# Kernel optimization log

Hardware: AMD Instinct MI355X
Metric: run time of the kernel (lower is better)

## Reference

```python
import jax, jax.numpy as jnp
import numpy as np

B, S, L, F, CD, NH, E, HID = 4, 1024, 256, 512, 768, 8, 8, 2048


def _xavier(k, shape):
    std = float(np.sqrt(1.0 / (shape[-2] + shape[-1])))
    return jax.random.normal(k, shape, dtype=jnp.float32) * std


def setup_inputs() -> dict:
    key = jax.random.key(0)
    ks = iter(jax.random.split(key, 64))
    nk = lambda: next(ks)
    inp = {}
    inp['x_r'] = jax.random.normal(nk(), (B, S, F), jnp.float32)
    inp['x_i'] = jax.random.normal(nk(), (B, S, F), jnp.float32)
    inp['ctx_r'] = jax.random.normal(nk(), (B, L, CD), jnp.float32)
    inp['ctx_i'] = jax.random.normal(nk(), (B, L, CD), jnp.float32)
    inp['ln1_g'] = jnp.ones((F,), jnp.float32)
    inp['ln2_g'] = jnp.ones((F,), jnp.float32)
    inp['ln3_g'] = jnp.ones((F,), jnp.float32)
    for pref, shp in [('sa_q', (F, F)), ('sa_k', (F, F)), ('sa_v', (F, F)), ('sa_o', (F, F)),
                      ('ca_q', (F, F)), ('ca_k', (CD, F)), ('ca_v', (CD, F)), ('ca_o', (F, F))]:
        inp[pref + 'Wr'] = _xavier(nk(), shp)
        inp[pref + 'Wi'] = _xavier(nk(), shp)
        inp[pref + 'br'] = jnp.zeros((F,), jnp.float32)
        inp[pref + 'bi'] = jnp.zeros((F,), jnp.float32)
    inp['moe_W1r'] = _xavier(nk(), (E, F, HID))
    inp['moe_W1i'] = _xavier(nk(), (E, F, HID))
    inp['moe_b1r'] = jnp.zeros((E, HID), jnp.float32)
    inp['moe_b1i'] = jnp.zeros((E, HID), jnp.float32)
    inp['moe_mb'] = jnp.zeros((E, HID), jnp.float32)  # modReLU bias
    inp['moe_W2r'] = _xavier(nk(), (E, HID, F))
    inp['moe_W2i'] = _xavier(nk(), (E, HID, F))
    inp['moe_b2r'] = jnp.zeros((E, F), jnp.float32)
    inp['moe_b2i'] = jnp.zeros((E, F), jnp.float32)
    return inp


def _clin(xr, xi, Wr, Wi, br, bi):
    # (xr + i xi) @ (Wr + i Wi) + (br + i bi)
    return xr @ Wr - xi @ Wi + br, xr @ Wi + xi @ Wr + bi


def _cln(xr, xi, g, eps=1e-6):
    amp = jnp.sqrt(xr * xr + xi * xi + eps)
    s = g * (amp / (jnp.mean(amp, axis=-1, keepdims=True) + eps)) / (amp + eps)
    return xr * s, xi * s


def _modrelu(xr, xi, b, eps=1e-10):
    amp = jnp.sqrt(xr * xr + xi * xi + eps)
    s = jax.nn.relu(amp + b) / (amp + eps)
    return xr * s, xi * s


def _cattn(xr, xi, cr, ci, qWr, qWi, qbr, qbi, kWr, kWi, kbr, kbi,
           vWr, vWi, vbr, vbi, oWr, oWi, obr, obi, nh):
    qr, qi = _clin(xr, xi, qWr, qWi, qbr, qbi)
    kr, ki = _clin(cr, ci, kWr, kWi, kbr, kbi)
    vr, vi = _clin(cr, ci, vWr, vWi, vbr, vbi)
    Bt, Sq, Ft = qr.shape
    Sk = kr.shape[1]
    d = Ft // nh
    sp = lambda t: t.reshape(Bt, t.shape[1], nh, d).transpose(0, 2, 1, 3)  # b n s d
    Qr, Qi, Kr, Ki, Vr, Vi = sp(qr), sp(qi), sp(kr), sp(ki), sp(vr), sp(vi)
    scale = 1.0 / float(d) ** 0.5
    scores = (jnp.einsum('bnqd,bnkd->bnqk', Qr, Kr)
              + jnp.einsum('bnqd,bnkd->bnqk', Qi, Ki)) * scale
    w = jax.nn.softmax(scores, axis=-1)
    mix = lambda t: jnp.einsum('bnqk,bnkd->bnqd', w, t).transpose(0, 2, 1, 3).reshape(Bt, Sq, Ft)
    return _clin(mix(Vr), mix(Vi), oWr, oWi, obr, obi)


def reference(x_r, x_i, ctx_r, ctx_i, ln1_g, ln2_g, ln3_g,
              sa_qWr, sa_qWi, sa_qbr, sa_qbi, sa_kWr, sa_kWi, sa_kbr, sa_kbi,
              sa_vWr, sa_vWi, sa_vbr, sa_vbi, sa_oWr, sa_oWi, sa_obr, sa_obi,
              ca_qWr, ca_qWi, ca_qbr, ca_qbi, ca_kWr, ca_kWi, ca_kbr, ca_kbi,
              ca_vWr, ca_vWi, ca_vbr, ca_vbi, ca_oWr, ca_oWi, ca_obr, ca_obi,
              moe_W1r, moe_W1i, moe_b1r, moe_b1i, moe_mb,
              moe_W2r, moe_W2i, moe_b2r, moe_b2i):
    # self-attention block
    hr, hi = _cln(x_r, x_i, ln1_g)
    ar, ai = _cattn(hr, hi, hr, hi, sa_qWr, sa_qWi, sa_qbr, sa_qbi,
                    sa_kWr, sa_kWi, sa_kbr, sa_kbi, sa_vWr, sa_vWi, sa_vbr, sa_vbi,
                    sa_oWr, sa_oWi, sa_obr, sa_obi, NH)
    xr, xi = x_r + ar, x_i + ai
    # cross-attention block
    hr, hi = _cln(xr, xi, ln2_g)
    ar, ai = _cattn(hr, hi, ctx_r, ctx_i, ca_qWr, ca_qWi, ca_qbr, ca_qbi,
                    ca_kWr, ca_kWi, ca_kbr, ca_kbi, ca_vWr, ca_vWi, ca_vbr, ca_vbi,
                    ca_oWr, ca_oWi, ca_obr, ca_obi, NH)
    xr, xi = xr + ar, xi + ai
    # phase-routed MoE block
    hr, hi = _cln(xr, xi, ln3_g)
    phase = jnp.arctan2(hi, hr)
    token_phase = jnp.arctan2(jnp.mean(jnp.sin(phase), axis=-1),
                              jnp.mean(jnp.cos(phase), axis=-1))
    idx = jnp.clip(jnp.floor((token_phase + jnp.pi) / (2.0 * jnp.pi) * E).astype(jnp.int32), 0, E - 1)
    acc_r = jnp.zeros_like(hr)
    acc_i = jnp.zeros_like(hi)
    for e in range(E):  # dense-compute-then-mask, faithful to source
        ur, ui = _clin(hr, hi, moe_W1r[e], moe_W1i[e], moe_b1r[e], moe_b1i[e])
        ur, ui = _modrelu(ur, ui, moe_mb[e])
        yr, yi = _clin(ur, ui, moe_W2r[e], moe_W2i[e], moe_b2r[e], moe_b2i[e])
        m = (idx == e).astype(hr.dtype)[..., None]
        acc_r = acc_r + yr * m
        acc_i = acc_i + yi * m
    xr, xi = xr + acc_r, xi + acc_i
    return jnp.stack([xr, xi])  # [2, B, S, F] real/imag
```

## Files before the change

kernel.cpp:

```cpp
#include <hip/hip_runtime.h>
#include <hip/hip_bf16.h>
#include <math.h>


#define NTOK 4096
#define FF   512
#define CDIM 768
#define NEXP 8
#define HID  2048
#define TMAX128 40
#define NPAD128 (TMAX128 * 128)

typedef __hip_bfloat16 bf16;
typedef short bf16x8 __attribute__((ext_vector_type(8)));
typedef float f32x4  __attribute__((ext_vector_type(4)));

struct Ptr6 { const float* p[6]; };
struct WPackAll {
    const float* sR[8]; const float* sI[8];
    bf16* dR[8]; bf16* dI[8];
    int kdiv[8];
};

__device__ __forceinline__ short f2bf(float x) {
    unsigned u = __float_as_uint(x);
    unsigned r = (u + 0x7fff + ((u >> 16) & 1)) >> 16;
    return (short)r;
}
__device__ __forceinline__ float bf2f(short s) {
    return __uint_as_float(((unsigned)(unsigned short)s) << 16);
}
__device__ __forceinline__ void gload16(const void* g, void* l) {
    __builtin_amdgcn_global_load_lds(
        (const __attribute__((address_space(1))) unsigned int*)g,
        (__attribute__((address_space(3))) unsigned int*)l, 16, 0, 0);
}

__global__ __launch_bounds__(256)
void cln_expand(const float* __restrict__ xr, const float* __restrict__ xi,
                const float* __restrict__ g,
                bf16* __restrict__ dR, bf16* __restrict__ dI)
{
    long base = (long)blockIdx.x * FF;
    int t = threadIdx.x;
    int j0 = t, j1 = t + 256;
    float xr0 = xr[base + j0], xi0 = xi[base + j0];
    float xr1 = xr[base + j1], xi1 = xi[base + j1];
    float a0 = sqrtf(xr0 * xr0 + xi0 * xi0 + 1e-6f);
    float a1 = sqrtf(xr1 * xr1 + xi1 * xi1 + 1e-6f);
    float s = a0 + a1;
#pragma unroll
    for (int off = 32; off >= 1; off >>= 1) s += __shfl_xor(s, off);
    __shared__ float wsum[4];
    if ((t & 63) == 0) wsum[t >> 6] = s;
    __syncthreads();
    float mean = (wsum[0] + wsum[1] + wsum[2] + wsum[3]) * (1.0f / 512.0f);
    float d0 = g[j0] * (a0 / (mean + 1e-6f)) / (a0 + 1e-6f);
    float d1 = g[j1] * (a1 / (mean + 1e-6f)) / (a1 + 1e-6f);
    long d = (long)blockIdx.x * 1024;
    float h; bf16 hh;
    h = xr0 * d0; hh = __float2bfloat16(h);
    dR[d + j0] = hh; dR[d + 512 + j0] = __float2bfloat16(h - __bfloat162float(hh));
    h = xi0 * d0; hh = __float2bfloat16(h);
    dI[d + j0] = hh; dI[d + 512 + j0] = __float2bfloat16(h - __bfloat162float(hh));
    h = xr1 * d1; hh = __float2bfloat16(h);
    dR[d + j1] = hh; dR[d + 512 + j1] = __float2bfloat16(h - __bfloat162float(hh));
    h = xi1 * d1; hh = __float2bfloat16(h);
    dI[d + j1] = hh; dI[d + 512 + j1] = __float2bfloat16(h - __bfloat162float(hh));
}

__global__ __launch_bounds__(256)
void cln_route(const float* __restrict__ xr, const float* __restrict__ xi,
               const float* __restrict__ g,
               bf16* __restrict__ h3r, bf16* __restrict__ h3i,
               int* __restrict__ eidx)
{
    long base = (long)blockIdx.x * FF;
    int t = threadIdx.x;
    int j0 = t, j1 = t + 256;
    float xr0 = xr[base + j0], xi0 = xi[base + j0];
    float xr1 = xr[base + j1], xi1 = xi[base + j1];
    float a0 = sqrtf(xr0 * xr0 + xi0 * xi0 + 1e-6f);
    float a1 = sqrtf(xr1 * xr1 + xi1 * xi1 + 1e-6f);
    float s = a0 + a1;
#pragma unroll
    for (int off = 32; off >= 1; off >>= 1) s += __shfl_xor(s, off);
    __shared__ float wsum[4];
    __shared__ double wss[4], wcc[4];
    if ((t & 63) == 0) wsum[t >> 6] = s;
    __syncthreads();
    float mean = (wsum[0] + wsum[1] + wsum[2] + wsum[3]) * (1.0f / 512.0f);
    float d0 = g[j0] * (a0 / (mean + 1e-6f)) / (a0 + 1e-6f);
    float d1 = g[j1] * (a1 / (mean + 1e-6f)) / (a1 + 1e-6f);
    float h0r = xr0 * d0, h0i = xi0 * d0;
    float h1r = xr1 * d1, h1i = xi1 * d1;
    h3r[base + j0] = __float2bfloat16(h0r);
    h3i[base + j0] = __float2bfloat16(h0i);
    h3r[base + j1] = __float2bfloat16(h1r);
    h3i[base + j1] = __float2bfloat16(h1i);
    float ph0 = atan2f(h0i, h0r), ph1 = atan2f(h1i, h1r);
    double ss = (double)sinf(ph0) + (double)sinf(ph1);
    double cc = (double)cosf(ph0) + (double)cosf(ph1);
#pragma unroll
    for (int off = 32; off >= 1; off >>= 1) {
        ss += __shfl_xor(ss, off);
        cc += __shfl_xor(cc, off);
    }
    if ((t & 63) == 0) { wss[t >> 6] = ss; wcc[t >> 6] = cc; }
    __syncthreads();
    if (t == 0) {
        float msin = (float)((wss[0] + wss[1] + wss[2] + wss[3]) * (1.0 / 512.0));
        float mcos = (float)((wcc[0] + wcc[1] + wcc[2] + wcc[3]) * (1.0 / 512.0));
        float tp = atan2f(msin, mcos);
        float a = (tp + 3.14159274101257324f) / 6.28318548202514648f * 8.0f;
        int k = (int)floorf(a);
        k = min(max(k, 0), NEXP - 1);
        eidx[blockIdx.x] = k;
    }
}

__global__ __launch_bounds__(256)
void expandA_x2(const float* __restrict__ sR, const float* __restrict__ sI,
                bf16* __restrict__ dR, bf16* __restrict__ dI, int K)
{
    int k = blockIdx.x * 256 + threadIdx.x;
    int m = blockIdx.y;
    long s = (long)m * K + k;
    long d = (long)m * 2 * K + k;
    float a = sR[s];
    bf16 ah = __float2bfloat16(a);
    dR[d] = ah; dR[d + K] = __float2bfloat16(a - __bfloat162float(ah));
    float b = sI[s];
    bf16 bh = __float2bfloat16(b);
    dI[d] = bh; dI[d + K] = __float2bfloat16(b - __bfloat162float(bh));
}

__global__ __launch_bounds__(256)
void expandW_all(WPackAll p)
{
    int z = blockIdx.z;
    int kdiv = p.kdiv[z];
    int kc = blockIdx.y;
    if (kc >= 2 * kdiv) return;
    const int N = FF;
    int g = blockIdx.x * 256 + threadIdx.x;
    int nt = g >> 6, l = g & 63;
    int lo = (kc >= kdiv);
    int kb = (kc - (lo ? kdiv : 0)) * 32 + (l >> 4) * 8;
    int n  = nt * 16 + (l & 15);
    long dbase = ((long)kc * (N >> 4) + nt) * 512 + l * 8;
    const float* sR = p.sR[z]; const float* sI = p.sI[z];
    bf16* dR = p.dR[z]; bf16* dI = p.dI[z];
#pragma unroll
    for (int j = 0; j < 8; j++) {
        float a = sR[(long)(kb + j) * N + n];
        bf16 ah = __float2bfloat16(a);
        dR[dbase + j] = lo ? __float2bfloat16(a - __bfloat162float(ah)) : ah;
        float b = sI[(long)(kb + j) * N + n];
        bf16 bh = __float2bfloat16(b);
        dI[dbase + j] = lo ? __float2bfloat16(b - __bfloat162float(bh)) : bh;
    }
}

__global__ __launch_bounds__(256)
void convW_packed(const float* __restrict__ sR, const float* __restrict__ sI,
                  bf16* __restrict__ dR, bf16* __restrict__ dI,
                  int N, long estride)
{
    int g = blockIdx.x * 256 + threadIdx.x;
    int nt = g >> 6, l = g & 63;
    int kc = blockIdx.y;
    int e  = blockIdx.z;
    const float* srcR = sR + (long)e * estride;
    const float* srcI = sI + (long)e * estride;
    bf16* dstR = dR + (long)e * estride;
    bf16* dstI = dI + (long)e * estride;
    int kb = kc * 32 + (l >> 4) * 8;
    int n  = nt * 16 + (l & 15);
    long dbase = ((long)kc * (N >> 4) + nt) * 512 + l * 8;
#pragma unroll
    for (int j = 0; j < 8; j++) {
        dstR[dbase + j] = __float2bfloat16(srcR[(long)(kb + j) * N + n]);
        dstI[dbase + j] = __float2bfloat16(srcI[(long)(kb + j) * N + n]);
    }
}

template<bool X3, bool EXPERT, bool GATHER, bool MODRELU, bool OUTBF16>
__global__ __launch_bounds__(256, 2)
void cgemm128(const bf16* __restrict__ Ar, const bf16* __restrict__ Ai,
              int lda, int Kreal,
              const bf16* __restrict__ Wr0, const bf16* __restrict__ Wi0,
              long wz, long westride, int ntTot, int kdiv,
              Ptr6 bias, int bstride, const float* __restrict__ mb,
              void* __restrict__ Cr0, void* __restrict__ Ci0, long cz,
              int ldc, int Kp,
              const int* __restrict__ order, const int* __restrict__ tileExpert)
{
    __shared__ short sA[16384];
    __shared__ short sW[16384];
    int tm = blockIdx.x, tn = blockIdx.y, z = blockIdx.z;
    const bf16* Wr = Wr0 + (long)z * wz;
    const bf16* Wi = Wi0 + (long)z * wz;
    const float* br = bias.p[2 * z];
    const float* bi = bias.p[2 * z + 1];
    void* Crv = (char*)Cr0 + (long)z * cz;
    void* Civ = (char*)Ci0 + (long)z * cz;
    if (EXPERT) {
        int e = tileExpert[tm];
        if (e < 0) return;
        Wr += (long)e * westride;  Wi += (long)e * westride;
        br += (long)e * bstride;   bi += (long)e * bstride;
        if (MODRELU) mb += (long)e * bstride;
    }
    int t = threadIdx.x;
    int l = t & 63, w = t >> 6;
    int riS = w >> 1, kcS = w & 1;
    const bf16* Asrc = riS ? Ai : Ar;
    const bf16* Wsrc = riS ? Wi : Wr;
    int kq8 = (l >> 4) * 8;
    long arb[8];
#pragma unroll
    for (int mt = 0; mt < 8; mt++) {
        int grow = tm * 128 + mt * 16 + (l & 15);
        int tok = grow;
        if (GATHER) { int gg = order[grow]; tok = (gg < 0) ? 0 : gg; }
        arb[mt] = (long)tok * lda;
    }
    int wm = w & 1, wn = w >> 1;

    f32x4 zf = {0.f, 0.f, 0.f, 0.f};
    f32x4 accR[4][4], accI[4][4];
#pragma unroll
    for (int a = 0; a < 4; a++)
#pragma unroll
        for (int b = 0; b < 4; b++) { accR[a][b] = zf; accI[a][b] = zf; }

    const bf16x8 sgn = {(short)0x8000,(short)0x8000,(short)0x8000,(short)0x8000,
                        (short)0x8000,(short)0x8000,(short)0x8000,(short)0x8000};

    for (int k0 = 0; k0 < Kp; k0 += 64) {
        __syncthreads();
        int lc = k0 + kcS * 32;
        int acol = (X3 && lc >= 2 * Kreal) ? lc - 2 * Kreal : lc;
#pragma unroll
        for (int mt = 0; mt < 8; mt++)
            gload16(Asrc + arb[mt] + acol + kq8,
                    &sA[(((riS * 2 + kcS) * 8 + mt) << 9)]);
        int kcl = (k0 >> 5) + kcS;
        int pkc = (X3 && kcl >= kdiv) ? kcl - kdiv : kcl;
        const bf16* wb = Wsrc + (((long)pkc * ntTot + tn * 8) << 9) + l * 8;
#pragma unroll
        for (int ntl = 0; ntl < 8; ntl++)
            gload16(wb + (ntl << 9),
                    &sW[(((riS * 2 + kcS) * 8 + ntl) << 9)]);
        __syncthreads();
#pragma unroll
        for (int kc = 0; kc < 2; kc++) {
            bf16x8 wrf[4], wif[4];
#pragma unroll
            for (int sn = 0; sn < 4; sn++) {
                wrf[sn] = *(const bf16x8*)&sW[(((kc * 8) + wn * 4 + sn) << 9) + l * 8];
                wif[sn] = *(const bf16x8*)&sW[((((2 + kc) * 8) + wn * 4 + sn) << 9) + l * 8];
            }
#pragma unroll
            for (int sm = 0; sm < 4; sm++) {
                bf16x8 ar = *(const bf16x8*)&sA[(((kc * 8) + wm * 4 + sm) << 9) + l * 8];
                bf16x8 ai = *(const bf16x8*)&sA[((((2 + kc) * 8) + wm * 4 + sm) << 9) + l * 8];
                bf16x8 na = ai ^ sgn;
#pragma unroll
                for (int sn = 0; sn < 4; sn++) {
                    accR[sm][sn] = __builtin_amdgcn_mfma_f32_16x16x32_bf16(ar, wrf[sn], accR[sm][sn], 0, 0, 0);
                    accR[sm][sn] = __builtin_amdgcn_mfma_f32_16x16x32_bf16(na, wif[sn], accR[sm][sn], 0, 0, 0);
                    accI[sm][sn] = __builtin_amdgcn_mfma_f32_16x16x32_bf16(ar, wif[sn], accI[sm][sn], 0, 0, 0);
                    accI[sm][sn] = __builtin_amdgcn_mfma_f32_16x16x32_bf16(ai, wrf[sn], accI[sm][sn], 0, 0, 0);
                }
            }
        }
    }
#pragma unroll
    for (int sm = 0; sm < 4; sm++)
#pragma unroll
        for (int sn = 0; sn < 4; sn++) {
            int row0 = tm * 128 + wm * 64 + sm * 16 + (l >> 4) * 4;
            int col  = tn * 128 + wn * 64 + sn * 16 + (l & 15);
            float bre = br[col], bie = bi[col];
            float mbe = MODRELU ? mb[col] : 0.f;
#pragma unroll
            for (int v = 0; v < 4; v++) {
                int row = row0 + v;
                float vr = accR[sm][sn][v] + bre;
                float vi = accI[sm][sn][v] + bie;
                if (MODRELU) {
                    float amp = sqrtf(vr * vr + vi * vi + 1e-10f);
                    float sc = fmaxf(amp + mbe, 0.f) / (amp + 1e-10f);
                    vr *= sc; vi *= sc;
                }
                long cidx = (long)row * ldc + col;
                if (OUTBF16) {
                    ((bf16*)Crv)[cidx] = __float2bfloat16(vr);
                    ((bf16*)Civ)[cidx] = __float2bfloat16(vi);
                } else {
                    ((float*)Crv)[cidx] = vr;
                    ((float*)Civ)[cidx] = vi;
                }
            }
        }
}

template<bool X3, bool EXPERT, bool GATHER, bool MODRELU, bool RESID, bool OUTBF16>
__global__ __launch_bounds__(256)
void cgemm_mfma(const bf16* __restrict__ Ar, const bf16* __restrict__ Ai,
                int lda, int Kreal,
                const bf16* __restrict__ Wr0, const bf16* __restrict__ Wi0,
                long wz, long westride, int ntTot, int kdiv,
                Ptr6 bias, int bstride, const float* __restrict__ mb,
                const float* __restrict__ Rr, const float* __restrict__ Ri,
                void* __restrict__ Cr0, void* __restrict__ Ci0, long cz,
                int ldc, int Kp,
                const int* __restrict__ order, const int* __restrict__ tileExpert)
{
    __shared__ short sA[8192];
    __shared__ short sW[8192];
    int tm = blockIdx.x, tn = blockIdx.y, z = blockIdx.z;
    const bf16* Wr = Wr0 + (long)z * wz;
    const bf16* Wi = Wi0 + (long)z * wz;
    const float* br = bias.p[2 * z];
    const float* bi = bias.p[2 * z + 1];
    void* Crv = (char*)Cr0 + (long)z * cz;
    void* Civ = (char*)Ci0 + (long)z * cz;
    if (EXPERT) {
        int e = tileExpert[tm];
        if (e < 0) return;
        Wr += (long)e * westride;  Wi += (long)e * westride;
        br += (long)e * bstride;   bi += (long)e * bstride;
        if (MODRELU) mb += (long)e * bstride;
    }
    int t = threadIdx.x;
    int l = t & 63, jj = t >> 6;
    int riS = jj >> 1, kcS = jj & 1;
    const bf16* Asrc = riS ? Ai : Ar;
    const bf16* Wsrc = riS ? Wi : Wr;
    int kq8 = (l >> 4) * 8;
    long arb[4];
#pragma unroll
    for (int mt = 0; mt < 4; mt++) {
        int grow = tm * 64 + mt * 16 + (l & 15);
        int tok = grow;
        if (GATHER) { int gg = order[grow]; tok = (gg < 0) ? 0 : gg; }
        arb[mt] = (long)tok * lda;
    }
    int wm = jj & 1, wn = jj >> 1;

    f32x4 zf = {0.f, 0.f, 0.f, 0.f};
    f32x4 accR[2][2], accI[2][2];
#pragma unroll
    for (int a = 0; a < 2; a++)
#pragma unroll
        for (int b = 0; b < 2; b++) { accR[a][b] = zf; accI[a][b] = zf; }

    const bf16x8 sgn = {(short)0x8000,(short)0x8000,(short)0x8000,(short)0x8000,
                        (short)0x8000,(short)0x8000,(short)0x8000,(short)0x8000};

    for (int k0 = 0; k0 < Kp; k0 += 64) {
        __syncthreads();
        int lc = k0 + kcS * 32;
        int acol = (X3 && lc >= 2 * Kreal) ? lc - 2 * Kreal : lc;
#pragma unroll
        for (int mt = 0; mt < 4; mt++)
            gload16(Asrc + arb[mt] + acol + kq8,
                    &sA[(((riS * 2 + kcS) << 2) + mt) << 9]);
        int kcl = (k0 >> 5) + kcS;
        int pkc = (X3 && kcl >= kdiv) ? kcl - kdiv : kcl;
        const bf16* wbase = Wsrc + (((long)pkc * ntTot + tn * 4) << 9) + l * 8;
#pragma unroll
        for (int ntl = 0; ntl < 4; ntl++)
            gload16(wbase + (ntl << 9),
                    &sW[(((riS * 2 + kcS) << 2) + ntl) << 9]);
        __syncthreads();
#pragma unroll
        for (int kc = 0; kc < 2; kc++) {
            bf16x8 arf[2], aif[2], naf[2], wrf[2], wif[2];
#pragma unroll
            for (int s = 0; s < 2; s++) {
                arf[s] = *(const bf16x8*)&sA[(((kc << 2) + wm * 2 + s) << 9) + l * 8];
                aif[s] = *(const bf16x8*)&sA[((((2 + kc) << 2) + wm * 2 + s) << 9) + l * 8];
                naf[s] = aif[s] ^ sgn;
                wrf[s] = *(const bf16x8*)&sW[(((kc << 2) + wn * 2 + s) << 9) + l * 8];
                wif[s] = *(const bf16x8*)&sW[((((2 + kc) << 2) + wn * 2 + s) << 9) + l * 8];
            }
#pragma unroll
            for (int sm = 0; sm < 2; sm++)
#pragma unroll
                for (int sn = 0; sn < 2; sn++) {
                    accR[sm][sn] = __builtin_amdgcn_mfma_f32_16x16x32_bf16(arf[sm], wrf[sn], accR[sm][sn], 0, 0, 0);
                    accR[sm][sn] = __builtin_amdgcn_mfma_f32_16x16x32_bf16(naf[sm], wif[sn], accR[sm][sn], 0, 0, 0);
                    accI[sm][sn] = __builtin_amdgcn_mfma_f32_16x16x32_bf16(arf[sm], wif[sn], accI[sm][sn], 0, 0, 0);
                    accI[sm][sn] = __builtin_amdgcn_mfma_f32_16x16x32_bf16(aif[sm], wrf[sn], accI[sm][sn], 0, 0, 0);
                }
        }
    }
#pragma unroll
    for (int sm = 0; sm < 2; sm++)
#pragma unroll
        for (int sn = 0; sn < 2; sn++) {
            int row0 = tm * 64 + (wm * 2 + sm) * 16 + (l >> 4) * 4;
            int col  = tn * 64 + (wn * 2 + sn) * 16 + (l & 15);
            float bre = br[col], bie = bi[col];
            float mbe = MODRELU ? mb[col] : 0.f;
#pragma unroll
            for (int v = 0; v < 4; v++) {
                int row = row0 + v;
                float vr = accR[sm][sn][v] + bre;
                float vi = accI[sm][sn][v] + bie;
                if (MODRELU) {
                    float amp = sqrtf(vr * vr + vi * vi + 1e-10f);
                    float sc = fmaxf(amp + mbe, 0.f) / (amp + 1e-10f);
                    vr *= sc; vi *= sc;
                }
                long cidx = (long)row * ldc + col;
                if (RESID) { vr += Rr[cidx]; vi += Ri[cidx]; }
                if (OUTBF16) {
                    ((bf16*)Crv)[cidx] = __float2bfloat16(vr);
                    ((bf16*)Civ)[cidx] = __float2bfloat16(vi);
                } else {
                    ((float*)Crv)[cidx] = vr;
                    ((float*)Civ)[cidx] = vi;
                }
            }
        }
}

__global__ __launch_bounds__(256)
void pack_kv(const float* __restrict__ kr, const float* __restrict__ ki,
             const float* __restrict__ vr, const float* __restrict__ vi,
             short* __restrict__ pK, short* __restrict__ pV, int Sk)
{
    const int F = FF;
    int kt = blockIdx.x, h = blockIdx.y, b = blockIdx.z;
    int nkt = gridDim.x;
    long blkbase = ((long)((b * 8 + h) * nkt) + kt) * 8192;
    int t = threadIdx.x;
#pragma unroll
    for (int it = 0; it < 2; it++) {
        int s = t + 256 * it;
        int sl = s & 63, g = s >> 6;
        int ri = g >> 2, c = (g >> 1) & 1, nt = g & 1;
        int sq = sl >> 4, sn = sl & 15;
        const float* src = ri ? ki : kr;
        long base = ((long)(b * Sk + kt * 32 + nt * 16 + sn)) * F + h * 64 + c * 32 + sq * 8;
        long outH = blkbase + ((((ri * 2 + 0) * 2 + c) * 2 + nt) * 64 + sl) * 8;
        long outL = blkbase + ((((ri * 2 + 1) * 2 + c) * 2 + nt) * 64 + sl) * 8;
#pragma unroll
        for (int j = 0; j < 8; j++) {
            float x = src[base + j];
            short xh = f2bf(x);
            pK[outH + j] = xh;
            pK[outL + j] = f2bf(x - bf2f(xh));
        }
    }
#pragma unroll
    for (int it = 0; it < 2; it++) {
        int s = t + 256 * it;
        int sl = s & 63, g = s >> 6;
        int ri = g >> 2, nt = g & 3;
        int sq = sl >> 4, sn = sl & 15;
        const float* src = ri ? vi : vr;
        long base = ((long)(b * Sk + kt * 32 + sq * 8)) * F + h * 64 + nt * 16 + sn;
        long outH = blkbase + (((ri * 2 + 0) * 4 + nt) * 64 + sl) * 8;
        long outL = blkbase + (((ri * 2 + 1) * 4 + nt) * 64 + sl) * 8;
#pragma unroll
        for (int j = 0; j < 8; j++) {
            float x = src[base + (long)j * F];
            short xh = f2bf(x);
            pV[outH + j] = xh;
            pV[outL + j] = f2bf(x - bf2f(xh));
        }
    }
}

__global__ __launch_bounds__(256)
void cattn_mfma(const float* __restrict__ qr, const float* __restrict__ qi,
                const short* __restrict__ pK, const short* __restrict__ pV,
                bf16* __restrict__ dR, bf16* __restrict__ dI,
                int S, int Sk)
{
    __shared__ short sK[8192];
    __shared__ short sV[8192];
    __shared__ short sP[5120];
    const int F = FF;
    int qt = blockIdx.x, h = blockIdx.y, b = blockIdx.z;
    int t = threadIdx.x;
    int w = t >> 6, l = t & 63, q = l >> 4, n16 = l & 15;

    bf16x8 qh_[2][2], ql_[2][2];
    {
        long qbase = ((long)(b * S + qt * 64 + w * 16 + n16)) * F + h * 64 + q * 8;
#pragma unroll
        for (int ri = 0; ri < 2; ri++) {
            const float* src = ri ? qi : qr;
#pragma unroll
            for (int c = 0; c < 2; c++) {
                float vv[8];
                *(float4*)&vv[0] = *(const float4*)&src[qbase + c * 32];
                *(float4*)&vv[4] = *(const float4*)&src[qbase + c * 32 + 4];
#pragma unroll
                for (int j = 0; j < 8; j++) {
                    short xh = f2bf(vv[j]);
                    qh_[ri][c][j] = xh;
                    ql_[ri][c][j] = f2bf(vv[j] - bf2f(xh));
                }
            }
        }
    }

    f32x4 zf = {0.f, 0.f, 0.f, 0.f};
    f32x4 oR[4], oI[4];
#pragma unroll
    for (int nt = 0; nt < 4; nt++) { oR[nt] = zf; oI[nt] = zf; }
    float m_run[4] = {-3.0e38f, -3.0e38f, -3.0e38f, -3.0e38f};
    float l_run[4] = {0.f, 0.f, 0.f, 0.f};

    int nkt = Sk >> 5;
    long pbh = (long)((b * 8 + h) * nkt) * 8192;
    for (int kt = 0; kt < nkt; kt++) {
        __syncthreads();
        long pb = pbh + (long)kt * 8192;
#pragma unroll
        for (int i = 0; i < 4; i++) {
            int bk = w * 4 + i;
            gload16(pK + pb + (bk << 9) + l * 8, &sK[bk << 9]);
            gload16(pV + pb + (bk << 9) + l * 8, &sV[bk << 9]);
        }
        __syncthreads();

        f32x4 sc[2];
        sc[0] = zf; sc[1] = zf;
#pragma unroll
        for (int nt = 0; nt < 2; nt++) {
#pragma unroll
            for (int ri = 0; ri < 2; ri++) {
                bf16x8 kh0 = *(const bf16x8*)&sK[((((ri * 2 + 0) * 2 + 0) * 2 + nt) * 64 + l) * 8];
                bf16x8 kh1 = *(const bf16x8*)&sK[((((ri * 2 + 0) * 2 + 1) * 2 + nt) * 64 + l) * 8];
                bf16x8 kl0 = *(const bf16x8*)&sK[((((ri * 2 + 1) * 2 + 0) * 2 + nt) * 64 + l) * 8];
                bf16x8 kl1 = *(const bf16x8*)&sK[((((ri * 2 + 1) * 2 + 1) * 2 + nt) * 64 + l) * 8];
                sc[nt] = __builtin_amdgcn_mfma_f32_16x16x32_bf16(qh_[ri][0], kh0, sc[nt], 0, 0, 0);
                sc[nt] = __builtin_amdgcn_mfma_f32_16x16x32_bf16(qh_[ri][1], kh1, sc[nt], 0, 0, 0);
                sc[nt] = __builtin_amdgcn_mfma_f32_16x16x32_bf16(ql_[ri][0], kh0, sc[nt], 0, 0, 0);
                sc[nt] = __builtin_amdgcn_mfma_f32_16x16x32_bf16(ql_[ri][1], kh1, sc[nt], 0, 0, 0);
                sc[nt] = __builtin_amdgcn_mfma_f32_16x16x32_bf16(qh_[ri][0], kl0, sc[nt], 0, 0, 0);
                sc[nt] = __builtin_amdgcn_mfma_f32_16x16x32_bf16(qh_[ri][1], kl1, sc[nt], 0, 0, 0);
            }
        }
        float alpha[4];
#pragma unroll
        for (int v = 0; v < 4; v++) {
            float s0 = sc[0][v] * 0.125f, s1 = sc[1][v] * 0.125f;
            float mx = fmaxf(s0, s1);
            mx = fmaxf(mx, __shfl_xor(mx, 1));
            mx = fmaxf(mx, __shfl_xor(mx, 2));
            mx = fmaxf(mx, __shfl_xor(mx, 4));
            mx = fmaxf(mx, __shfl_xor(mx, 8));
            float mnew = fmaxf(m_run[v], mx);
            float p0 = __expf(s0 - mnew), p1 = __expf(s1 - mnew);
            sc[0][v] = p0; sc[1][v] = p1;
            float ps = p0 + p1;
            ps += __shfl_xor(ps, 1);
            ps += __shfl_xor(ps, 2);
            ps += __shfl_xor(ps, 4);
            ps += __shfl_xor(ps, 8);
            alpha[v] = __expf(m_run[v] - mnew);
            l_run[v] = l_run[v] * alpha[v] + ps;
            m_run[v] = mnew;
        }
#pragma unroll
        for (int nt = 0; nt < 4; nt++)
#pragma unroll
            for (int v = 0; v < 4; v++) { oR[nt][v] *= alpha[v]; oI[nt][v] *= alpha[v]; }
        int pbase = w * 1280;
#pragma unroll
        for (int nt = 0; nt < 2; nt++)
#pragma unroll
            for (int v = 0; v < 4; v++) {
                float p = sc[nt][v];
                short ph = f2bf(p);
                short pl = f2bf(p - bf2f(ph));
                int idx = pbase + (q * 4 + v) * 40 + nt * 16 + n16;
                sP[idx] = ph;
                sP[idx + 640] = pl;
            }
        bf16x8 pH = *(const bf16x8*)&sP[pbase + n16 * 40 + q * 8];
        bf16x8 pL = *(const bf16x8*)&sP[pbase + 640 + n16 * 40 + q * 8];
#pragma unroll
        for (int nt = 0; nt < 4; nt++) {
            bf16x8 vh = *(const bf16x8*)&sV[(((0 * 2 + 0) * 4 + nt) * 64 + l) * 8];
            bf16x8 vl = *(const bf16x8*)&sV[(((0 * 2 + 1) * 4 + nt) * 64 + l) * 8];
            oR[nt] = __builtin_amdgcn_mfma_f32_16x16x32_bf16(pH, vh, oR[nt], 0, 0, 0);
            oR[nt] = __builtin_amdgcn_mfma_f32_16x16x32_bf16(pL, vh, oR[nt], 0, 0, 0);
            oR[nt] = __builtin_amdgcn_mfma_f32_16x16x32_bf16(pH, vl, oR[nt], 0, 0, 0);
            bf16x8 wh = *(const bf16x8*)&sV[(((1 * 2 + 0) * 4 + nt) * 64 + l) * 8];
            bf16x8 wl2 = *(const bf16x8*)&sV[(((1 * 2 + 1) * 4 + nt) * 64 + l) * 8];
            oI[nt] = __builtin_amdgcn_mfma_f32_16x16x32_bf16(pH, wh, oI[nt], 0, 0, 0);
            oI[nt] = __builtin_amdgcn_mfma_f32_16x16x32_bf16(pL, wh, oI[nt], 0, 0, 0);
            oI[nt] = __builtin_amdgcn_mfma_f32_16x16x32_bf16(pH, wl2, oI[nt], 0, 0, 0);
        }
    }
#pragma unroll
    for (int v = 0; v < 4; v++) {
        float inv = 1.0f / l_run[v];
        long rbase = ((long)(b * S + qt * 64 + w * 16 + q * 4 + v)) * 1024;
#pragma unroll
        for (int nt = 0; nt < 4; nt++) {
            int col = h * 64 + nt * 16 + n16;
            float vr = oR[nt][v] * inv;
            bf16 hh = __float2bfloat16(vr);
            dR[rbase + col] = hh;
            dR[rbase + 512 + col] = __float2bfloat16(vr - __bfloat162float(hh));
            float vi = oI[nt][v] * inv;
            bf16 hi2 = __float2bfloat16(vi);
            dI[rbase + col] = hi2;
            dI[rbase + 512 + col] = __float2bfloat16(vi - __bfloat162float(hi2));
        }
    }
}

__global__ __launch_bounds__(256)
void moe_build_kernel(const int* __restrict__ eidx, int* __restrict__ order,
                      int* __restrict__ te128, int* __restrict__ te64)
{
    __shared__ int cnt[NEXP], segbase[NEXP], cursor[NEXP], tb128[NEXP], n128[NEXP];
    int t = threadIdx.x;
    if (t < NEXP) { cnt[t] = 0; cursor[t] = 0; }
    __syncthreads();
    for (int i = t; i < NTOK; i += 256) atomicAdd(&cnt[eidx[i]], 1);
    __syncthreads();
    if (t == 0) {
        int ob = 0, tb = 0;
        for (int e = 0; e < NEXP; e++) {
            segbase[e] = ob; tb128[e] = tb;
            int tiles = (cnt[e] + 127) >> 7;
            n128[e] = tiles;
            ob += tiles << 7; tb += tiles;
        }
    }
    __syncthreads();
    for (int i = t; i < NPAD128; i += 256) order[i] = -1;
    if (t < TMAX128) {
        int ex = -1;
        for (int e = 0; e < NEXP; e++)
            if (t >= tb128[e] && t < tb128[e] + n128[e]) ex = e;
        te128[t] = ex;
    }
    if (t >= 64 && t < 64 + 2 * TMAX128) {
        int tt = t - 64;
        int ex = -1;
        for (int e = 0; e < NEXP; e++)
            if (tt >= tb128[e] * 2 && tt < (tb128[e] + n128[e]) * 2) ex = e;
        te64[tt] = ex;
    }
    __syncthreads();
    for (int i = t; i < NTOK; i += 256) {
        int e = eidx[i];
        int pos = atomicAdd(&cursor[e], 1);
        order[segbase[e] + pos] = i;
    }
}

__global__ __launch_bounds__(256)
void combine_kernel(const int* __restrict__ order,
                    const float* __restrict__ xr, const float* __restrict__ xi,
                    const float* __restrict__ yr, const float* __restrict__ yi,
                    float* __restrict__ out)
{
    const int F = FF;
    int p = blockIdx.x;
    int tok = order[p];
    if (tok < 0) return;
    int t = threadIdx.x;
    float* outr = out;
    float* outi = out + (long)NTOK * FF;
#pragma unroll
    for (int u = 0; u < 2; u++) {
        int j = t + u * 256;
        long src = (long)p * F + j;
        long dst = (long)tok * F + j;
        outr[dst] = xr[dst] + yr[src];
        outi[dst] = xi[dst] + yi[src];
    }
}

extern "C" void kernel_launch(void* const* d_in, const int* in_sizes, int n_in,
                              void* d_out, int out_size, void* d_ws, size_t ws_size,
                              hipStream_t stream)
{
    (void)in_sizes; (void)n_in; (void)out_size; (void)ws_size;
    const float* x_r   = (const float*)d_in[0];
    const float* x_i   = (const float*)d_in[1];
    const float* ctx_r = (const float*)d_in[2];
    const float* ctx_i = (const float*)d_in[3];
    const float* ln1_g = (const float*)d_in[4];
    const float* ln2_g = (const float*)d_in[5];
    const float* ln3_g = (const float*)d_in[6];
    const float* sa_qWr = (const float*)d_in[7];   const float* sa_qWi = (const float*)d_in[8];
    const float* sa_qbr = (const float*)d_in[9];   const float* sa_qbi = (const float*)d_in[10];
    const float* sa_kWr = (const float*)d_in[11];  const float* sa_kWi = (const float*)d_in[12];
    const float* sa_kbr = (const float*)d_in[13];  const float* sa_kbi = (const float*)d_in[14];
    const float* sa_vWr = (const float*)d_in[15];  const float* sa_vWi = (const float*)d_in[16];
    const float* sa_vbr = (const float*)d_in[17];  const float* sa_vbi = (const float*)d_in[18];
    const float* sa_oWr = (const float*)d_in[19];  const float* sa_oWi = (const float*)d_in[20];
    const float* sa_obr = (const float*)d_in[21];  const float* sa_obi = (const float*)d_in[22];
    const float* ca_qWr = (const float*)d_in[23];  const float* ca_qWi = (const float*)d_in[24];
    const float* ca_qbr = (const float*)d_in[25];  const float* ca_qbi = (const float*)d_in[26];
    const float* ca_kWr = (const float*)d_in[27];  const float* ca_kWi = (const float*)d_in[28];
    const float* ca_kbr = (const float*)d_in[29];  const float* ca_kbi = (const float*)d_in[30];
    const float* ca_vWr = (const float*)d_in[31];  const float* ca_vWi = (const float*)d_in[32];
    const float* ca_vbr = (const float*)d_in[33];  const float* ca_vbi = (const float*)d_in[34];
    const float* ca_oWr = (const float*)d_in[35];  const float* ca_oWi = (const float*)d_in[36];
    const float* ca_obr = (const float*)d_in[37];  const float* ca_obi = (const float*)d_in[38];
    const float* moe_W1r = (const float*)d_in[39]; const float* moe_W1i = (const float*)d_in[40];
    const float* moe_b1r = (const float*)d_in[41]; const float* moe_b1i = (const float*)d_in[42];
    const float* moe_mb  = (const float*)d_in[43];
    const float* moe_W2r = (const float*)d_in[44]; const float* moe_W2i = (const float*)d_in[45];
    const float* moe_b2r = (const float*)d_in[46]; const float* moe_b2i = (const float*)d_in[47];
    float* out = (float*)d_out;

    char* W = (char*)d_ws;
    const long NF = (long)NTOK * FF;
    const long NF4 = NF * 4;
    float* xr = (float*)(W + 0 * NF4);
    float* xi = (float*)(W + 1 * NF4);
    char* base2 = W + 2 * NF4;
    short* pKbuf = (short*)base2;
    bf16* h3r = (bf16*)base2;
    bf16* h3i = (bf16*)(base2 + 4194304);
    char* poolB = W + 4 * NF4;
    float* qr = (float*)poolB;                float* qi = (float*)(poolB + NF4);
    float* kr = (float*)(poolB + 2 * NF4);    float* ki = (float*)(poolB + 3 * NF4);
    float* vr = (float*)(poolB + 4 * NF4);    float* vi = (float*)(poolB + 5 * NF4);
    short* pVbuf = (short*)(poolB + 6 * NF4);
    bf16* u_r = (bf16*)poolB;
    bf16* u_i = (bf16*)(poolB + 20971520);
    float* y_r = (float*)(poolB + 41943040);
    float* y_i = (float*)(poolB + 52428800);
    char* Q = W + 12 * NF4;
    bf16* A1r = (bf16*)Q;
    bf16* A1i = (bf16*)(Q + 8388608);
    bf16* A2r = (bf16*)(Q + 16777216);
    bf16* A2i = (bf16*)(Q + 19922944);
    char* WQ = Q + 23068672;
    const long PS1 = 524288;
    const long PS2 = 786432;
    bf16* saq_r = (bf16*)(WQ);                   bf16* saq_i = saq_r + PS1;
    bf16* sak_r = saq_r + 2 * PS1;               bf16* sak_i = saq_r + 3 * PS1;
    bf16* sav_r = saq_r + 4 * PS1;               bf16* sav_i = saq_r + 5 * PS1;
    bf16* sao_r = saq_r + 6 * PS1;               bf16* sao_i = saq_r + 7 * PS1;
    bf16* caq_r = saq_r + 8 * PS1;               bf16* caq_i = saq_r + 9 * PS1;
    bf16* cao_r = saq_r + 10 * PS1;              bf16* cao_i = saq_r + 11 * PS1;
    bf16* cak_r = saq_r + 12 * PS1;              bf16* cak_i = cak_r + PS2;
    bf16* cav_r = cak_r + 2 * PS2;               bf16* cav_i = cak_r + 3 * PS2;
    bf16* Wm_r = (bf16*)Q;
    bf16* Wm_i = (bf16*)(Q + 16777216);
    char* ints = W + 12 * NF4 + 41943040 + 524288;
    int* eidx  = (int*)ints;
    int* order = eidx + NTOK;
    int* te128 = order + NPAD128;
    int* te64  = te128 + 64;

    dim3 blk(256);
    const long W1S = (long)FF * HID;
    const long CZ = 2 * NF4;
    Ptr6 bQKV = {{sa_qbr, sa_qbi, sa_kbr, sa_kbi, sa_vbr, sa_vbi}};
    Ptr6 bSAO = {{sa_obr, sa_obi, 0, 0, 0, 0}};
    Ptr6 bCAQ = {{ca_qbr, ca_qbi, 0, 0, 0, 0}};
    Ptr6 bCKV = {{ca_kbr, ca_kbi, ca_vbr, ca_vbi, 0, 0}};
    Ptr6 bCAO = {{ca_obr, ca_obi, 0, 0, 0, 0}};
    Ptr6 bM1  = {{moe_b1r, moe_b1i, 0, 0, 0, 0}};
    Ptr6 bM2  = {{moe_b2r, moe_b2i, 0, 0, 0, 0}};

    WPackAll wp;
    wp.sR[0]=sa_qWr; wp.sI[0]=sa_qWi; wp.dR[0]=saq_r; wp.dI[0]=saq_i; wp.kdiv[0]=16;
    wp.sR[1]=sa_kWr; wp.sI[1]=sa_kWi; wp.dR[1]=sak_r; wp.dI[1]=sak_i; wp.kdiv[1]=16;
    wp.sR[2]=sa_vWr; wp.sI[2]=sa_vWi; wp.dR[2]=sav_r; wp.dI[2]=sav_i; wp.kdiv[2]=16;
    wp.sR[3]=sa_oWr; wp.sI[3]=sa_oWi; wp.dR[3]=sao_r; wp.dI[3]=sao_i; wp.kdiv[3]=16;
    wp.sR[4]=ca_qWr; wp.sI[4]=ca_qWi; wp.dR[4]=caq_r; wp.dI[4]=caq_i; wp.kdiv[4]=16;
    wp.sR[5]=ca_oWr; wp.sI[5]=ca_oWi; wp.dR[5]=cao_r; wp.dI[5]=cao_i; wp.kdiv[5]=16;
    wp.sR[6]=ca_kWr; wp.sI[6]=ca_kWi; wp.dR[6]=cak_r; wp.dI[6]=cak_i; wp.kdiv[6]=24;
    wp.sR[7]=ca_vWr; wp.sI[7]=ca_vWi; wp.dR[7]=cav_r; wp.dI[7]=cav_i; wp.kdiv[7]=24;
    expandW_all<<<dim3(8, 48, 8), blk, 0, stream>>>(wp);

    cln_expand<<<NTOK, blk, 0, stream>>>(x_r, x_i, ln1_g, A1r, A1i);
    cgemm128<true,false,false,false,false><<<dim3(32, 4, 3), blk, 0, stream>>>(
        A1r, A1i, 1024, 512, saq_r, saq_i, 2 * PS1, 0, 32, 16,
        bQKV, 0, nullptr, qr, qi, CZ, FF, 1536, nullptr, nullptr);
    pack_kv<<<dim3(32, 8, 4), blk, 0, stream>>>(kr, ki, vr, vi, pKbuf, pVbuf, 1024);
    cattn_mfma<<<dim3(16, 8, 4), blk, 0, stream>>>(qr, qi, pKbuf, pVbuf, A1r, A1i, 1024, 1024);
    cgemm_mfma<true,false,false,false,true,false><<<dim3(64, 8, 1), blk, 0, stream>>>(
        A1r, A1i, 1024, 512, sao_r, sao_i, 0, 0, 32, 16,
        bSAO, 0, nullptr, x_r, x_i, xr, xi, 0, FF, 1536, nullptr, nullptr);

    cln_expand<<<NTOK, blk, 0, stream>>>(xr, xi, ln2_g, A1r, A1i);
    cgemm_mfma<true,false,false,false,false,false><<<dim3(64, 8, 1), blk, 0, stream>>>(
        A1r, A1i, 1024, 512, caq_r, caq_i, 0, 0, 32, 16,
        bCAQ, 0, nullptr, nullptr, nullptr, qr, qi, 0, FF, 1536, nullptr, nullptr);
    expandA_x2<<<dim3(3, 1024), blk, 0, stream>>>(ctx_r, ctx_i, A2r, A2i, CDIM);
    cgemm_mfma<true,false,false,false,false,false><<<dim3(16, 8, 2), blk, 0, stream>>>(
        A2r, A2i, 1536, 768, cak_r, cak_i, 2 * PS2, 0, 32, 24,
        bCKV, 0, nullptr, nullptr, nullptr, kr, ki, CZ, FF, 2304, nullptr, nullptr);
    pack_kv<<<dim3(8, 8, 4), blk, 0, stream>>>(kr, ki, vr, vi, pKbuf, pVbuf, 256);
    cattn_mfma<<<dim3(16, 8, 4), blk, 0, stream>>>(qr, qi, pKbuf, pVbuf, A1r, A1i, 1024, 256);
    cgemm_mfma<true,false,false,false,true,false><<<dim3(64, 8, 1), blk, 0, stream>>>(
        A1r, A1i, 1024, 512, cao_r, cao_i, 0, 0, 32, 16,
        bCAO, 0, nullptr, xr, xi, xr, xi, 0, FF, 1536, nullptr, nullptr);

    cln_route<<<NTOK, blk, 0, stream>>>(xr, xi, ln3_g, h3r, h3i, eidx);
    moe_build_kernel<<<1, blk, 0, stream>>>(eidx, order, te128, te64);
    convW_packed<<<dim3(32, 16, 8), blk, 0, stream>>>(moe_W1r, moe_W1i, Wm_r, Wm_i, HID, W1S);
    cgemm128<false,true,true,true,true><<<dim3(TMAX128, 16, 1), blk, 0, stream>>>(
        h3r, h3i, 512, 512, Wm_r, Wm_i, 0, W1S, 128, 0,
        bM1, HID, moe_mb, u_r, u_i, 0, HID, 512, order, te128);
    convW_packed<<<dim3(8, 64, 8), blk, 0, stream>>>(moe_W2r, moe_W2i, Wm_r, Wm_i, FF, W1S);
    cgemm_mfma<false,true,false,false,false,false><<<dim3(2 * TMAX128, 8, 1), blk, 0, stream>>>(
        u_r, u_i, 2048, 2048, Wm_r, Wm_i, 0, W1S, 32, 0,
        bM2, FF, nullptr, nullptr, nullptr, y_r, y_i, 0, FF, 2048, nullptr, te64);
    combine_kernel<<<NPAD128, blk, 0, stream>>>(order, xr, xi, y_r, y_i, out);
}
```

Measured before the change: 866.5 us.

## Remap GEMM and attention blocks per XCD; use 128-tile GEMM for MoE down-projection

Adds an XCD-aware block index remap to cgemm128 and cattn_mfma, so blocks that share weight tiles or K/V heads land on the same XCD and its L2 cache. The MoE second GEMM switches from the 64-row cgemm_mfma to the 128-row cgemm128 with a 1D grid of 160 blocks and the 128-row tile-expert map. The aim is better L2 reuse and fewer weight reloads. The cost is less parallelism for the down-projection, since it now launches 160 blocks, and the remap assumes a fixed grid shape.

```diff
diff --git a/kernel.cpp b/kernel.cpp
--- a/kernel.cpp
+++ b/kernel.cpp
@@ -193,12 +193,21 @@
               long wz, long westride, int ntTot, int kdiv,
               Ptr6 bias, int bstride, const float* __restrict__ mb,
               void* __restrict__ Cr0, void* __restrict__ Ci0, long cz,
-              int ldc, int Kp,
+              int ldc, int Kp, int bandM,
               const int* __restrict__ order, const int* __restrict__ tileExpert)
 {
     __shared__ short sA[16384];
     __shared__ short sW[16384];
-    int tm = blockIdx.x, tn = blockIdx.y, z = blockIdx.z;
+    int tm, tn, z;
+    if (bandM > 0) {
+        int L = blockIdx.x;
+        int xcd = L & 7, idx = L >> 3;
+        tm = xcd * bandM + idx % bandM;
+        tn = idx / bandM;
+        z = 0;
+    } else {
+        tm = blockIdx.x; tn = blockIdx.y; z = blockIdx.z;
+    }
     const bf16* Wr = Wr0 + (long)z * wz;
     const bf16* Wi = Wi0 + (long)z * wz;
     const float* br = bias.p[2 * z];
@@ -488,7 +497,11 @@
     __shared__ short sV[8192];
     __shared__ short sP[5120];
     const int F = FF;
-    int qt = blockIdx.x, h = blockIdx.y, b = blockIdx.z;
+    int L = blockIdx.x;
+    int xcd = L & 7, idx = L >> 3;
+    int bh = xcd * 4 + (idx & 3);
+    int qt = idx >> 2;
+    int b = bh >> 3, h = bh & 7;
     int t = threadIdx.x;
     int w = t >> 6, l = t & 63, q = l >> 4, n16 = l & 15;
 
@@ -584,9 +597,9 @@
                 float p = sc[nt][v];
                 short ph = f2bf(p);
                 short pl = f2bf(p - bf2f(ph));
-                int idx = pbase + (q * 4 + v) * 40 + nt * 16 + n16;
-                sP[idx] = ph;
-                sP[idx + 640] = pl;
+                int idxp = pbase + (q * 4 + v) * 40 + nt * 16 + n16;
+                sP[idxp] = ph;
+                sP[idxp + 640] = pl;
             }
         bf16x8 pH = *(const bf16x8*)&sP[pbase + n16 * 40 + q * 8];
         bf16x8 pL = *(const bf16x8*)&sP[pbase + 640 + n16 * 40 + q * 8];
@@ -790,9 +803,9 @@
     cln_expand<<<NTOK, blk, 0, stream>>>(x_r, x_i, ln1_g, A1r, A1i);
     cgemm128<true,false,false,false,false><<<dim3(32, 4, 3), blk, 0, stream>>>(
         A1r, A1i, 1024, 512, saq_r, saq_i, 2 * PS1, 0, 32, 16,
-        bQKV, 0, nullptr, qr, qi, CZ, FF, 1536, nullptr, nullptr);
+        bQKV, 0, nullptr, qr, qi, CZ, FF, 1536, 0, nullptr, nullptr);
     pack_kv<<<dim3(32, 8, 4), blk, 0, stream>>>(kr, ki, vr, vi, pKbuf, pVbuf, 1024);
-    cattn_mfma<<<dim3(16, 8, 4), blk, 0, stream>>>(qr, qi, pKbuf, pVbuf, A1r, A1i, 1024, 1024);
+    cattn_mfma<<<512, blk, 0, stream>>>(qr, qi, pKbuf, pVbuf, A1r, A1i, 1024, 1024);
     cgemm_mfma<true,false,false,false,true,false><<<dim3(64, 8, 1), blk, 0, stream>>>(
         A1r, A1i, 1024, 512, sao_r, sao_i, 0, 0, 32, 16,
         bSAO, 0, nullptr, x_r, x_i, xr, xi, 0, FF, 1536, nullptr, nullptr);
@@ -806,7 +819,7 @@
         A2r, A2i, 1536, 768, cak_r, cak_i, 2 * PS2, 0, 32, 24,
         bCKV, 0, nullptr, nullptr, nullptr, kr, ki, CZ, FF, 2304, nullptr, nullptr);
     pack_kv<<<dim3(8, 8, 4), blk, 0, stream>>>(kr, ki, vr, vi, pKbuf, pVbuf, 256);
-    cattn_mfma<<<dim3(16, 8, 4), blk, 0, stream>>>(qr, qi, pKbuf, pVbuf, A1r, A1i, 1024, 256);
+    cattn_mfma<<<512, blk, 0, stream>>>(qr, qi, pKbuf, pVbuf, A1r, A1i, 1024, 256);
     cgemm_mfma<true,false,false,false,true,false><<<dim3(64, 8, 1), blk, 0, stream>>>(
         A1r, A1i, 1024, 512, cao_r, cao_i, 0, 0, 32, 16,
         bCAO, 0, nullptr, xr, xi, xr, xi, 0, FF, 1536, nullptr, nullptr);
@@ -814,12 +827,12 @@
     cln_route<<<NTOK, blk, 0, stream>>>(xr, xi, ln3_g, h3r, h3i, eidx);
     moe_build_kernel<<<1, blk, 0, stream>>>(eidx, order, te128, te64);
     convW_packed<<<dim3(32, 16, 8), blk, 0, stream>>>(moe_W1r, moe_W1i, Wm_r, Wm_i, HID, W1S);
-    cgemm128<false,true,true,true,true><<<dim3(TMAX128, 16, 1), blk, 0, stream>>>(
+    cgemm128<false,true,true,true,true><<<640, blk, 0, stream>>>(
         h3r, h3i, 512, 512, Wm_r, Wm_i, 0, W1S, 128, 0,
-        bM1, HID, moe_mb, u_r, u_i, 0, HID, 512, order, te128);
+        bM1, HID, moe_mb, u_r, u_i, 0, HID, 512, 5, order, te128);
     convW_packed<<<dim3(8, 64, 8), blk, 0, stream>>>(moe_W2r, moe_W2i, Wm_r, Wm_i, FF, W1S);
-    cgemm_mfma<false,true,false,false,false,false><<<dim3(2 * TMAX128, 8, 1), blk, 0, stream>>>(
+    cgemm128<false,true,false,false,false><<<160, blk, 0, stream>>>(
         u_r, u_i, 2048, 2048, Wm_r, Wm_i, 0, W1S, 32, 0,
-        bM2, FF, nullptr, nullptr, nullptr, y_r, y_i, 0, FF, 2048, nullptr, te64);
+        bM2, FF, nullptr, y_r, y_i, 0, FF, 2048, 5, nullptr, te128);
     combine_kernel<<<NPAD128, blk, 0, stream>>>(order, xr, xi, y_r, y_i, out);
 }
```

New measurement: 866.4 us. About the same (-0.0%).
